# Optimization experiments

Hardware: AMD Instinct MI355X
Metric: run time of the kernel (lower is better)

The kernel has to match this reference:

```python
import jax, jax.numpy as jnp
import numpy as np

B, T, D, H, C = 32, 512, 768, 512, 7


def setup_inputs() -> dict:
    key = jax.random.key(0)
    ks = jax.random.split(key, 10)
    g = lambda k, shape: jax.random.normal(k, shape, jnp.float32) * 0.02
    return {
        "x": jax.random.normal(ks[0], (B, T, D), jnp.float32),
        # PyTorch LSTM params; b = b_ih + b_hh folded into one bias (same math)
        "Wf_ih": g(ks[1], (4 * H, 2 * D)),
        "Wf_hh": g(ks[2], (4 * H, H)),
        "bf": jnp.zeros((4 * H,), jnp.float32),
        "Wb_ih": g(ks[3], (4 * H, 2 * D)),
        "Wb_hh": g(ks[4], (4 * H, H)),
        "bb": jnp.zeros((4 * H,), jnp.float32),
        "W_enc": g(ks[5], (H, D)),
        "b_enc": jnp.zeros((H,), jnp.float32),
        "W_dec": g(ks[6], (H, H)),
        "b_dec": jnp.zeros((H,), jnp.float32),
        "v": jax.random.uniform(ks[7], (H,), jnpp := jnp.float32) if False else jax.random.uniform(ks[7], (H,), jnp.float32),
        "W_head": g(ks[8], (C, 2 * H)),
        "b_head": jnp.zeros((C,), jnp.float32),
    }


def reference(x, Wf_ih, Wf_hh, bf, Wb_ih, Wb_hh, bb, W_enc, b_enc, W_dec, b_dec, v, W_head, b_head):
    hid = W_dec.shape[0]
    # encoder projection is time-invariant -> hoist out of the loop (same math as original)
    enc_proj = jnp.einsum('btd,hd->bth', x, W_enc) + b_enc  # (B,T,H)

    def run_direction(x_seq, Wih, Whh, b):
        def step(carry, xt):
            h, c = carry                                    # (B,H) each
            dec = h @ W_dec.T + b_dec                       # (B,H)
            scores = jnp.tanh(enc_proj + dec[:, None, :]) @ v  # (B,T)
            w = jax.nn.softmax(scores, axis=1)
            ctx = jnp.einsum('bt,btd->bd', w, x)            # (B,D)
            inp = jnp.concatenate([ctx, xt], axis=1)        # (B,2D)
            gates = inp @ Wih.T + h @ Whh.T + b             # (B,4H), torch order i,f,g,o
            i_, f_, g_, o_ = jnp.split(gates, 4, axis=1)
            c = jax.nn.sigmoid(f_) * c + jax.nn.sigmoid(i_) * jnp.tanh(g_)
            h = jax.nn.sigmoid(o_) * jnp.tanh(c)
            return (h, c), h

        h0 = jnp.zeros((x.shape[0], hid), x.dtype)
        (_, _), hs = jax.lax.scan(step, (h0, h0), x_seq)
        return hs                                           # (T,B,H)

    x_seq = jnp.swapaxes(x, 0, 1)                           # (T,B,D)
    hs_f = run_direction(x_seq, Wf_ih, Wf_hh, bf)
    hs_b = run_direction(x_seq[::-1], Wb_ih, Wb_hh, bb)[::-1]
    comb = jnp.swapaxes(jnp.concatenate([hs_f, hs_b], axis=-1), 0, 1)  # (B,T,2H)
    return comb @ W_head.T + b_head                          # (B,T,C)
```

## Files before the change

kernel.cpp:

```cpp
#include <hip/hip_runtime.h>
#include <cstdint>
#include <cstddef>

#define L2E 1.4426950408889634f

typedef __attribute__((ext_vector_type(8))) short short8v;
typedef __attribute__((ext_vector_type(4))) float f32x4;
typedef unsigned long long ull;

__device__ __forceinline__ float fexp2(float x){ return __builtin_amdgcn_exp2f(x); }
__device__ __forceinline__ float frcp(float x){ return __builtin_amdgcn_rcpf(x); }
__device__ __forceinline__ float tanh_f(float x){
  return 1.f - 2.f*frcp(1.f + fexp2(2.f*L2E*x));
}
__device__ __forceinline__ float sigm_f(float x){
  return frcp(1.f + fexp2(-L2E*x));
}
__device__ __forceinline__ float bf2f(ushort u){ return __uint_as_float(((uint32_t)u)<<16); }
__device__ __forceinline__ ushort f2bf(float f){
  uint32_t x = __float_as_uint(f);
  uint32_t r = (x + 0x7FFFu + ((x>>16)&1u)) >> 16;
  return (ushort)r;
}

__device__ __forceinline__ float ld4f(const float* p){
  return __hip_atomic_load((float*)p, __ATOMIC_RELAXED, __HIP_MEMORY_SCOPE_AGENT);
}
__device__ __forceinline__ void st4f(float* p, float v){
  __hip_atomic_store(p, v, __ATOMIC_RELAXED, __HIP_MEMORY_SCOPE_AGENT);
}
__device__ __forceinline__ void st2h(ushort* p, ushort v){
  __hip_atomic_store(p, v, __ATOMIC_RELAXED, __HIP_MEMORY_SCOPE_AGENT);
}
__device__ __forceinline__ short8v ld16h(const ushort* p){
  union { ull u[2]; short8v s; } c;
  c.u[0] = __hip_atomic_load((ull*)p,     __ATOMIC_RELAXED, __HIP_MEMORY_SCOPE_AGENT);
  c.u[1] = __hip_atomic_load((ull*)(p+4), __ATOMIC_RELAXED, __HIP_MEMORY_SCOPE_AGENT);
  return c.s;
}
__device__ __forceinline__ void st8u(ushort* p, ull v){
  __hip_atomic_store((ull*)p, v, __ATOMIC_RELAXED, __HIP_MEMORY_SCOPE_AGENT);
}

namespace {
constexpr int NB = 32, TT = 512, DD = 768, HH = 512;
constexpr size_t EPB  = 0;
constexpr size_t XBB  = EPB  + (size_t)NB*HH*TT*2;
constexpr size_t HSB  = XBB  + (size_t)NB*TT*DD*2;
constexpr size_t WPKB = HSB  + (size_t)2*TT*NB*HH*2;
constexpr size_t WDPB = WPKB + (size_t)2*128*64*64*8*2;
constexpr size_t CTXB = WDPB + (size_t)32*16*64*8*2;
constexpr size_t CSTB = CTXB + (size_t)2*NB*DD*4;
constexpr size_t GSYB = CSTB + (size_t)2*NB*HH*4;
constexpr size_t WS_BYTES = GSYB + 32768;

constexpr int EPL  = 0;
constexpr int WPL  = 65536;
constexpr int REDL = 131072;
constexpr int HEVL = 147456;
constexpr int HBL  = 151680;
constexpr int DPL  = 153856;
constexpr int DECL = 155904;
constexpr int VVL  = 156416;
constexpr int CSCL = 156672;
constexpr int GFNL = 159776;
constexpr int LDS_BYTES = GFNL + 2176;
}

__device__ __forceinline__ void bar_arrive(uint* flags, uint token, int bid){
  __syncthreads();
  if (threadIdx.x == 0)
    __hip_atomic_store(&flags[bid*16], token, __ATOMIC_RELAXED, __HIP_MEMORY_SCOPE_AGENT);
}
__device__ __forceinline__ void bar_wait(uint* flags, uint token){
  if (threadIdx.x < 256) {
    while (__hip_atomic_load(&flags[threadIdx.x*16], __ATOMIC_RELAXED, __HIP_MEMORY_SCOPE_AGENT) < token)
      __builtin_amdgcn_s_sleep(1);
  }
  __syncthreads();
  asm volatile("" ::: "memory");
}

__global__ void k_xcast(const float* __restrict__ x, ushort* __restrict__ xb)
{
  size_t i = ((size_t)blockIdx.x*256 + threadIdx.x)*8;
  float4 v0 = *(const float4*)(x + i);
  float4 v1 = *(const float4*)(x + i + 4);
  short8v o;
  o[0]=(short)f2bf(v0.x); o[1]=(short)f2bf(v0.y); o[2]=(short)f2bf(v0.z); o[3]=(short)f2bf(v0.w);
  o[4]=(short)f2bf(v1.x); o[5]=(short)f2bf(v1.y); o[6]=(short)f2bf(v1.z); o[7]=(short)f2bf(v1.w);
  *(short8v*)(xb + i) = o;
}

__global__ void k_encproj(const float* __restrict__ x, const float* __restrict__ Wenc,
                          const float* __restrict__ benc, ushort* __restrict__ epT)
{
  int b = blockIdx.z, h0 = blockIdx.y*64, t0 = blockIdx.x*64;
  __shared__ float As[64][33];
  __shared__ float Bs[64][33];
  int tid = threadIdx.x;
  int n = tid & 63, mg = tid >> 6;
  float acc[16];
  #pragma unroll
  for (int j = 0; j < 16; j++) acc[j] = 0.f;
  int lr = tid >> 2, lk = (tid & 3) * 8;
  for (int k0 = 0; k0 < 768; k0 += 32) {
    const float* ap = Wenc + (size_t)(h0 + lr)*768 + k0 + lk;
    #pragma unroll
    for (int i = 0; i < 8; i++) As[lr][lk + i] = ap[i];
    const float* bp = x + ((size_t)b*512 + t0 + lr)*768 + k0 + lk;
    #pragma unroll
    for (int i = 0; i < 8; i++) Bs[lr][lk + i] = bp[i];
    __syncthreads();
    #pragma unroll
    for (int kk = 0; kk < 32; kk++) {
      float bv = Bs[n][kk];
      #pragma unroll
      for (int j = 0; j < 16; j++) acc[j] += As[mg*16 + j][kk] * bv;
    }
    __syncthreads();
  }
  #pragma unroll
  for (int j = 0; j < 16; j++) {
    int h = h0 + mg*16 + j;
    epT[((size_t)b*512 + h)*512 + t0 + n] = f2bf(acc[j] + benc[h]);
  }
}

__global__ void k_wpack(const float* __restrict__ Wfih, const float* __restrict__ Wfhh,
                        const float* __restrict__ Wbih, const float* __restrict__ Wbhh,
                        ushort* __restrict__ wpk)
{
  size_t f = (size_t)blockIdx.x*256 + threadIdx.x;
  int lane = (int)(f & 63), kstep = (int)((f>>6)&63), jblk = (int)((f>>12)&127), dir = (int)(f>>19);
  const float* Whh = dir ? Wbhh : Wfhh;
  const float* Wih = dir ? Wbih : Wfih;
  int c = lane & 15, gate = c >> 2, jj = c & 3;
  int row = gate*512 + jblk*4 + jj;
  int kbase = kstep*32 + (lane>>4)*8;
  short8v o;
  #pragma unroll
  for (int i = 0; i < 8; i++) {
    int k = kbase + i;
    float w = (k < 512) ? Whh[(size_t)row*512 + k] : Wih[(size_t)row*1536 + (k - 512)];
    o[i] = (short)f2bf(w);
  }
  *(short8v*)(wpk + f*8) = o;
}

__global__ void k_wdpack(const float* __restrict__ Wdec, ushort* __restrict__ wdp)
{
  int f = blockIdx.x*256 + threadIdx.x;
  int lane = f & 63, kstep = (f >> 6) & 15, nb = f >> 10;
  int n = nb*16 + (lane & 15);
  int kbase = kstep*32 + (lane >> 4)*8;
  short8v o;
  #pragma unroll
  for (int i = 0; i < 8; i++) o[i] = (short)f2bf(Wdec[(size_t)n*512 + kbase + i]);
  *(short8v*)(wdp + (size_t)f*8) = o;
}

__device__ __forceinline__ void gates_hx(int s, int wid, int lane, int l15, int lk8, int dirG,
    const ushort* __restrict__ hsb, const ushort* __restrict__ xb,
    const ushort* wpk_l, float* RED)
{
  if (wid >= 2 && wid <= 4) return;
  int b0 = l15, b1 = 16 + l15;
  f32x4 acc0 = {0,0,0,0}, acc1 = {0,0,0,0};
  if (wid < 2) {
    if (s > 0) {
      int t_prev = dirG ? (512 - s) : (s - 1);
      const ushort* h0 = hsb + (((size_t)dirG*512 + t_prev)*32 + b0)*512;
      const ushort* h1 = hsb + (((size_t)dirG*512 + t_prev)*32 + b1)*512;
      #pragma unroll
      for (int kk = 0; kk < 8; kk++) {
        int kstep = wid*8 + kk;
        int ko = kstep*32 + lk8;
        short8v a0v = *(const short8v*)(h0 + ko);
        short8v a1v = *(const short8v*)(h1 + ko);
        short8v bv  = *(const short8v*)(wpk_l + (size_t)kstep*512 + lane*8);
        acc0 = __builtin_amdgcn_mfma_f32_16x16x32_bf16(a0v, bv, acc0, 0, 0, 0);
        acc1 = __builtin_amdgcn_mfma_f32_16x16x32_bf16(a1v, bv, acc1, 0, 0, 0);
      }
    }
  } else {
    int t_in = dirG ? (511 - s) : s;
    const ushort* x0 = xb + ((size_t)b0*512 + t_in)*768;
    const ushort* x1 = xb + ((size_t)b1*512 + t_in)*768;
    #pragma unroll
    for (int kk = 0; kk < 8; kk++) {
      int kstep = wid*8 + kk;
      int ko = kstep*32 - 1280 + lk8;
      short8v a0v = *(const short8v*)(x0 + ko);
      short8v a1v = *(const short8v*)(x1 + ko);
      short8v bv  = *(const short8v*)(wpk_l + (size_t)kstep*512 + lane*8);
      acc0 = __builtin_amdgcn_mfma_f32_16x16x32_bf16(a0v, bv, acc0, 0, 0, 0);
      acc1 = __builtin_amdgcn_mfma_f32_16x16x32_bf16(a1v, bv, acc1, 0, 0, 0);
    }
  }
  int rr = (lane >> 4) * 4;
  #pragma unroll
  for (int r = 0; r < 4; r++) RED[((size_t)wid*32 + rr + r)*16 + l15] = acc0[r];
  #pragma unroll
  for (int r = 0; r < 4; r++) RED[((size_t)wid*32 + 16 + rr + r)*16 + l15] = acc1[r];
}

__global__ __launch_bounds__(512, 1) void k_loop(
    ushort* __restrict__ hsb, const ushort* __restrict__ xb, const ushort* __restrict__ ep,
    const ushort* __restrict__ wpk, const ushort* __restrict__ wdp,
    float* __restrict__ spart, ushort* __restrict__ ctxf,
    float* __restrict__ cst, const float* __restrict__ bdec, const float* __restrict__ vg,
    const float* __restrict__ bfv, const float* __restrict__ bbv,
    uint* __restrict__ flags, uint* __restrict__ gfl)
{
  extern __shared__ __align__(16) char dsm[];
  ushort* ep_l  = (ushort*)(dsm + EPL);
  ushort* wpk_l = (ushort*)(dsm + WPL);
  float*  RED   = (float*)(dsm + REDL);
  float*  HEV   = (float*)(dsm + HEVL);
  ushort* HB    = (ushort*)(dsm + HBL);
  float*  DP    = (float*)(dsm + DPL);
  float*  DEC   = (float*)(dsm + DECL);
  float*  VV    = (float*)(dsm + VVL);
  float*  CSC   = (float*)(dsm + CSCL);
  float*  GFIN  = (float*)(dsm + GFNL);

  const int bid = blockIdx.x;
  const int tid = threadIdx.x;
  const int wid = tid >> 6, lane = tid & 63;
  const int l15 = lane & 15, lk8 = (lane >> 4) * 8;
  const int bS = bid >> 3, hc = bid & 7;
  const int dirG = bid >> 7, jblkG = bid & 127;
  uint bar_t = 0;

  {
    const short8v* esrc = (const short8v*)(ep + ((size_t)bS*512 + hc*64)*512);
    short8v* edst = (short8v*)ep_l;
    for (int i = tid; i < 4096; i += 512) edst[i] = esrc[i];
    const short8v* wsrc = (const short8v*)(wpk + (((size_t)dirG*128 + jblkG)*64)*512);
    short8v* wdst = (short8v*)wpk_l;
    for (int i = tid; i < 4096; i += 512) wdst[i] = wsrc[i];
    if (tid < 64) VV[tid] = vg[hc*64 + tid];
  }
  ++bar_t; bar_arrive(flags, bar_t, bid); bar_wait(flags, bar_t);

  for (int s = 0; s < TT; ++s) {
    if (s == 0) {
      if (tid < 128) { int dir = tid >> 6, n = tid & 63; DEC[dir*64 + n] = bdec[hc*64 + n]; }
    } else {
      if (tid < 128) {
        int dir = tid >> 6, q = tid & 63;
        int tp = dir ? (512 - s) : (s - 1);
        short8v hv = *(const short8v*)(hsb + (((size_t)dir*512 + tp)*32 + bS)*512 + q*8);
        *(short8v*)&HB[(dir*4 + (q >> 4))*136 + (q & 15)*8] = hv;
      }
      __syncthreads();
      {
        int dir = tid >> 8, n = (tid >> 2) & 63, kq = tid & 3;
        int ng = hc*64 + n, nb = ng >> 4, c = ng & 15;
        const ushort* hrow = HB + (dir*4 + kq)*136;
        float a = 0.f;
        #pragma unroll
        for (int ch = 0; ch < 16; ch++) {
          int kstep = kq*4 + (ch >> 2), lhi = ch & 3;
          short8v w8 = *(const short8v*)(wdp + (((size_t)nb*16 + kstep)*64 + lhi*16 + c)*8);
          #pragma unroll
          for (int j = 0; j < 8; j++) a += bf2f((ushort)w8[j]) * bf2f(hrow[ch*8 + j]);
        }
        DP[tid] = a;
      }
      __syncthreads();
      if (tid < 128) {
        int dir = tid >> 6, n = tid & 63;
        const float* dp = DP + dir*256 + n*4;
        DEC[dir*64 + n] = dp[0] + dp[1] + dp[2] + dp[3] + bdec[hc*64 + n];
      }
    }
    __syncthreads();

    float s0 = 0.f, s1 = 0.f;
    {
      int t = tid;
      #pragma unroll 8
      for (int h = 0; h < 64; h++) {
        float e = bf2f(ep_l[h*512 + t]);
        float vv = VV[h];
        s0 += tanh_f(e + DEC[h]) * vv;
        s1 += tanh_f(e + DEC[64 + h]) * vv;
      }
    }

    {
      float* sp = spart + (((size_t)(bS*8 + hc))*2)*512;
      st4f(sp + tid, s0);
      st4f(sp + 512 + tid, s1);
      __syncthreads();
      if (tid == 0)
        __hip_atomic_store(&gfl[bid*16], (uint)(s + 1), __ATOMIC_RELAXED, __HIP_MEMORY_SCOPE_AGENT);
      if (tid < 8) {
        while (__hip_atomic_load(&gfl[(bS*8 + tid)*16], __ATOMIC_RELAXED, __HIP_MEMORY_SCOPE_AGENT) < (uint)(s + 1))
          __builtin_amdgcn_s_sleep(1);
      }
      __syncthreads();
      float s0r = 0.f, s1r = 0.f;
      #pragma unroll
      for (int j = 0; j < 8; j++) {
        const float* spj = spart + (((size_t)(bS*8 + j))*2)*512;
        s0r += ld4f(spj + tid);
        s1r += ld4f(spj + 512 + tid);
      }
      s0r = fminf(s0r, 100.f); s1r = fminf(s1r, 100.f);
      float e0 = fexp2((s0r - 32.f)*L2E);
      float e1 = fexp2((s1r - 32.f)*L2E);
      float z0 = e0, z1 = e1;
      #pragma unroll
      for (int off = 32; off; off >>= 1) { z0 += __shfl_xor(z0, off); z1 += __shfl_xor(z1, off); }
      if (lane == 0) { DP[wid] = z0; DP[8 + wid] = z1; }
      __syncthreads();
      if (tid < 2) {
        float z = 0.f;
        #pragma unroll
        for (int w = 0; w < 8; w++) z += DP[tid*8 + w];
        DP[128 + tid] = frcp(z);
      }
      __syncthreads();
      e0 *= DP[128]; e1 *= DP[129];
      HEV[(tid >> 7)*132 + (tid & 127)] = e0;
      HEV[(4 + (tid >> 7))*132 + (tid & 127)] = e1;
      __syncthreads();
    }

    if (tid < 384) {
      int dl = tid % 96, tq = tid / 96;
      const ushort* xp = xb + (((size_t)bS*512 + tq*128)*768) + hc*96 + dl;
      const float* ev0 = HEV + tq*132;
      const float* ev1 = HEV + (4 + tq)*132;
      float a0 = 0.f, a1 = 0.f;
      #pragma unroll 8
      for (int t2 = 0; t2 < 128; t2++) {
        float xv = bf2f(xp[(size_t)t2*768]);
        a0 += ev0[t2]*xv;
        a1 += ev1[t2]*xv;
      }
      CSC[(tq*2 + 0)*97 + dl] = a0;
      CSC[(tq*2 + 1)*97 + dl] = a1;
    }
    __syncthreads();
    if (tid < 192) {
      int dl = tid % 96, dir = tid / 96;
      float cv = CSC[(0*2 + dir)*97 + dl] + CSC[(1*2 + dir)*97 + dl]
               + CSC[(2*2 + dir)*97 + dl] + CSC[(3*2 + dir)*97 + dl];
      st2h(ctxf + ((size_t)dir*32 + bS)*768 + hc*96 + dl, f2bf(cv));
    }

    ++bar_t; bar_arrive(flags, bar_t, bid);
    gates_hx(s, wid, lane, l15, lk8, dirG, hsb, xb, wpk_l, RED);
    bar_wait(flags, bar_t);

    {
      if (wid >= 2 && wid <= 4) {
        int b0 = l15, b1 = 16 + l15;
        f32x4 acc0 = {0,0,0,0}, acc1 = {0,0,0,0};
        const ushort* c0 = ctxf + ((size_t)dirG*32 + b0)*768;
        const ushort* c1 = ctxf + ((size_t)dirG*32 + b1)*768;
        #pragma unroll
        for (int kk = 0; kk < 8; kk++) {
          int kstep = wid*8 + kk;
          int ko = kstep*32 - 512 + lk8;
          short8v a0v = ld16h(c0 + ko);
          short8v a1v = ld16h(c1 + ko);
          short8v bv  = *(const short8v*)(wpk_l + (size_t)kstep*512 + lane*8);
          acc0 = __builtin_amdgcn_mfma_f32_16x16x32_bf16(a0v, bv, acc0, 0, 0, 0);
          acc1 = __builtin_amdgcn_mfma_f32_16x16x32_bf16(a1v, bv, acc1, 0, 0, 0);
        }
        int rr = (lane >> 4) * 4;
        #pragma unroll
        for (int r = 0; r < 4; r++) RED[((size_t)wid*32 + rr + r)*16 + l15] = acc0[r];
        #pragma unroll
        for (int r = 0; r < 4; r++) RED[((size_t)wid*32 + 16 + rr + r)*16 + l15] = acc1[r];
      }
      __syncthreads();
      {
        int bb = tid >> 4, c = tid & 15;
        float g = 0.f;
        #pragma unroll
        for (int w = 0; w < 8; w++) g += RED[((size_t)w*32 + bb)*16 + c];
        GFIN[bb*17 + c] = g;
      }
      __syncthreads();
      if (tid < 32) {
        int b = tid;
        int j0 = jblkG*4;
        const float* bias = dirG ? bbv : bfv;
        size_t ci0 = ((size_t)dirG*32 + b)*512 + j0;
        float4 co = *(const float4*)&cst[ci0];
        float cold[4] = {co.x, co.y, co.z, co.w};
        float4 cn4;
        ull hp = 0;
        #pragma unroll
        for (int jj = 0; jj < 4; jj++) {
          int j = j0 + jj;
          float gi  = GFIN[b*17 + jj]       + bias[j];
          float gf  = GFIN[b*17 + 4 + jj]   + bias[512 + j];
          float gg  = GFIN[b*17 + 8 + jj]   + bias[1024 + j];
          float go_ = GFIN[b*17 + 12 + jj]  + bias[1536 + j];
          float cn = sigm_f(gf)*cold[jj] + sigm_f(gi)*tanh_f(gg);
          float h  = sigm_f(go_)*tanh_f(cn);
          ((float*)&cn4)[jj] = cn;
          hp |= ((ull)f2bf(h)) << (16*jj);
        }
        *(float4*)&cst[ci0] = cn4;
        int tw = dirG ? (511 - s) : s;
        st8u(hsb + (((size_t)dirG*512 + tw)*32 + b)*512 + j0, hp);
      }
    }
    ++bar_t; bar_arrive(flags, bar_t, bid);
    bar_wait(flags, bar_t);
  }
}

__global__ void k_head(const ushort* __restrict__ hsb, const float* __restrict__ Wh,
                       const float* __restrict__ bh, float* __restrict__ out)
{
  int wid = threadIdx.x >> 6, lane = threadIdx.x & 63;
  int r = blockIdx.x*4 + wid;
  int b = r >> 9, t = r & 511;
  float acc[7];
  #pragma unroll
  for (int c = 0; c < 7; c++) acc[c] = 0.f;
  const ushort* hf = hsb + (((size_t)t)*32 + b)*512;
  const ushort* hb = hsb + (((size_t)512 + t)*32 + b)*512;
  for (int k0 = 0; k0 < 512; k0 += 64) {
    int k = k0 + lane;
    float a = bf2f(hf[k]), bvv = bf2f(hb[k]);
    #pragma unroll
    for (int c = 0; c < 7; c++)
      acc[c] += a*Wh[c*1024 + k] + bvv*Wh[c*1024 + 512 + k];
  }
  #pragma unroll
  for (int c = 0; c < 7; c++) {
    float sres = acc[c];
    #pragma unroll
    for (int off = 32; off; off >>= 1) sres += __shfl_xor(sres, off);
    if (lane == c) out[((size_t)b*512 + t)*7 + c] = sres + bh[c];
  }
}

extern "C" void kernel_launch(void* const* d_in, const int* in_sizes, int n_in,
                              void* d_out, int out_size, void* d_ws, size_t ws_size,
                              hipStream_t stream) {
  (void)in_sizes; (void)n_in; (void)out_size;
  const float* x    = (const float*)d_in[0];
  const float* Wfih = (const float*)d_in[1];
  const float* Wfhh = (const float*)d_in[2];
  const float* bfv  = (const float*)d_in[3];
  const float* Wbih = (const float*)d_in[4];
  const float* Wbhh = (const float*)d_in[5];
  const float* bbv  = (const float*)d_in[6];
  const float* Wenc = (const float*)d_in[7];
  const float* benc = (const float*)d_in[8];
  const float* Wdec = (const float*)d_in[9];
  const float* bdec = (const float*)d_in[10];
  const float* v    = (const float*)d_in[11];
  const float* Whead= (const float*)d_in[12];
  const float* bhead= (const float*)d_in[13];
  float* out = (float*)d_out;
  char* ws = (char*)d_ws;

  if (ws_size < WS_BYTES) return;

  ushort* ep   = (ushort*)(ws + EPB);
  float*  spart= (float*)(ws + EPB);
  ushort* xb   = (ushort*)(ws + XBB);
  ushort* hsb  = (ushort*)(ws + HSB);
  ushort* wpk  = (ushort*)(ws + WPKB);
  ushort* wdp  = (ushort*)(ws + WDPB);
  ushort* ctxf = (ushort*)(ws + CTXB);
  float*  cst  = (float*)(ws + CSTB);
  uint*   flags= (uint*)(ws + GSYB);
  uint*   gfl  = (uint*)(ws + GSYB + 16384);

  hipFuncSetAttribute(reinterpret_cast<const void*>(k_loop),
                      hipFuncAttributeMaxDynamicSharedMemorySize, LDS_BYTES);

  hipMemsetAsync(ws + CSTB, 0, (size_t)2*NB*HH*4, stream);
  hipMemsetAsync(ws + GSYB, 0, 32768, stream);

  hipLaunchKernelGGL(k_xcast, dim3(6144), dim3(256), 0, stream, x, xb);
  hipLaunchKernelGGL(k_encproj, dim3(8,8,32), dim3(256), 0, stream, x, Wenc, benc, ep);
  hipLaunchKernelGGL(k_wpack, dim3(4096), dim3(256), 0, stream, Wfih, Wfhh, Wbih, Wbhh, wpk);
  hipLaunchKernelGGL(k_wdpack, dim3(128), dim3(256), 0, stream, Wdec, wdp);

  void* args[] = {
    (void*)&hsb, (void*)&xb, (void*)&ep, (void*)&wpk, (void*)&wdp,
    (void*)&spart, (void*)&ctxf, (void*)&cst,
    (void*)&bdec, (void*)&v, (void*)&bfv, (void*)&bbv,
    (void*)&flags, (void*)&gfl
  };
  hipLaunchCooperativeKernel(reinterpret_cast<void*>(k_loop), dim3(256), dim3(512),
                             args, LDS_BYTES, stream);

  hipLaunchKernelGGL(k_head, dim3(4096), dim3(256), 0, stream, hsb, Whead, bhead, out);
}
```

Measured before the change: 14.01 ms.

## Split gate GEMM into h and x parts and overlap each with barrier waits

The fused h/x gate GEMM is split into two functions. The input-x contribution for step s+1 is now computed while waiting on the end-of-step grid barrier, including once before the loop for step 0. The recurrent h contribution is computed while waiting on the score-partial flags, with the spin-waiting threads moved to wave 2 so waves 0-1 can run the MFMAs. The aim is to hide GEMM latency behind the grid-wide synchronisation stalls. It relies on RED slots for x and h waves not being overwritten between producer and consumer across barriers.

Result: slower. 14.87 ms (+6.2%).

```diff
diff --git a/kernel.cpp b/kernel.cpp
--- a/kernel.cpp
+++ b/kernel.cpp
@@ -160,43 +160,52 @@
   *(short8v*)(wdp + (size_t)f*8) = o;
 }
 
-__device__ __forceinline__ void gates_hx(int s, int wid, int lane, int l15, int lk8, int dirG,
-    const ushort* __restrict__ hsb, const ushort* __restrict__ xb,
-    const ushort* wpk_l, float* RED)
-{
-  if (wid >= 2 && wid <= 4) return;
+__device__ __forceinline__ void gates_h(int s, int wid, int lane, int l15, int lk8, int dirG,
+    const ushort* __restrict__ hsb, const ushort* wpk_l, float* RED)
+{
+  if (wid >= 2) return;
   int b0 = l15, b1 = 16 + l15;
   f32x4 acc0 = {0,0,0,0}, acc1 = {0,0,0,0};
-  if (wid < 2) {
-    if (s > 0) {
-      int t_prev = dirG ? (512 - s) : (s - 1);
-      const ushort* h0 = hsb + (((size_t)dirG*512 + t_prev)*32 + b0)*512;
-      const ushort* h1 = hsb + (((size_t)dirG*512 + t_prev)*32 + b1)*512;
-      #pragma unroll
-      for (int kk = 0; kk < 8; kk++) {
-        int kstep = wid*8 + kk;
-        int ko = kstep*32 + lk8;
-        short8v a0v = *(const short8v*)(h0 + ko);
-        short8v a1v = *(const short8v*)(h1 + ko);
-        short8v bv  = *(const short8v*)(wpk_l + (size_t)kstep*512 + lane*8);
-        acc0 = __builtin_amdgcn_mfma_f32_16x16x32_bf16(a0v, bv, acc0, 0, 0, 0);
-        acc1 = __builtin_amdgcn_mfma_f32_16x16x32_bf16(a1v, bv, acc1, 0, 0, 0);
-      }
-    }
-  } else {
-    int t_in = dirG ? (511 - s) : s;
-    const ushort* x0 = xb + ((size_t)b0*512 + t_in)*768;
-    const ushort* x1 = xb + ((size_t)b1*512 + t_in)*768;
+  if (s > 0) {
+    int t_prev = dirG ? (512 - s) : (s - 1);
+    const ushort* h0 = hsb + (((size_t)dirG*512 + t_prev)*32 + b0)*512;
+    const ushort* h1 = hsb + (((size_t)dirG*512 + t_prev)*32 + b1)*512;
     #pragma unroll
     for (int kk = 0; kk < 8; kk++) {
       int kstep = wid*8 + kk;
-      int ko = kstep*32 - 1280 + lk8;
-      short8v a0v = *(const short8v*)(x0 + ko);
-      short8v a1v = *(const short8v*)(x1 + ko);
+      int ko = kstep*32 + lk8;
+      short8v a0v = *(const short8v*)(h0 + ko);
+      short8v a1v = *(const short8v*)(h1 + ko);
       short8v bv  = *(const short8v*)(wpk_l + (size_t)kstep*512 + lane*8);
       acc0 = __builtin_amdgcn_mfma_f32_16x16x32_bf16(a0v, bv, acc0, 0, 0, 0);
       acc1 = __builtin_amdgcn_mfma_f32_16x16x32_bf16(a1v, bv, acc1, 0, 0, 0);
     }
+  }
+  int rr = (lane >> 4) * 4;
+  #pragma unroll
+  for (int r = 0; r < 4; r++) RED[((size_t)wid*32 + rr + r)*16 + l15] = acc0[r];
+  #pragma unroll
+  for (int r = 0; r < 4; r++) RED[((size_t)wid*32 + 16 + rr + r)*16 + l15] = acc1[r];
+}
+
+__device__ __forceinline__ void gates_x(int s, int wid, int lane, int l15, int lk8, int dirG,
+    const ushort* __restrict__ xb, const ushort* wpk_l, float* RED)
+{
+  if (wid < 5) return;
+  int b0 = l15, b1 = 16 + l15;
+  f32x4 acc0 = {0,0,0,0}, acc1 = {0,0,0,0};
+  int t_in = dirG ? (511 - s) : s;
+  const ushort* x0 = xb + ((size_t)b0*512 + t_in)*768;
+  const ushort* x1 = xb + ((size_t)b1*512 + t_in)*768;
+  #pragma unroll
+  for (int kk = 0; kk < 8; kk++) {
+    int kstep = wid*8 + kk;
+    int ko = kstep*32 - 1280 + lk8;
+    short8v a0v = *(const short8v*)(x0 + ko);
+    short8v a1v = *(const short8v*)(x1 + ko);
+    short8v bv  = *(const short8v*)(wpk_l + (size_t)kstep*512 + lane*8);
+    acc0 = __builtin_amdgcn_mfma_f32_16x16x32_bf16(a0v, bv, acc0, 0, 0, 0);
+    acc1 = __builtin_amdgcn_mfma_f32_16x16x32_bf16(a1v, bv, acc1, 0, 0, 0);
   }
   int rr = (lane >> 4) * 4;
   #pragma unroll
@@ -242,7 +251,9 @@
     for (int i = tid; i < 4096; i += 512) wdst[i] = wsrc[i];
     if (tid < 64) VV[tid] = vg[hc*64 + tid];
   }
-  ++bar_t; bar_arrive(flags, bar_t, bid); bar_wait(flags, bar_t);
+  ++bar_t; bar_arrive(flags, bar_t, bid);
+  gates_x(0, wid, lane, l15, lk8, dirG, xb, wpk_l, RED);
+  bar_wait(flags, bar_t);
 
   for (int s = 0; s < TT; ++s) {
     if (s == 0) {
@@ -297,8 +308,9 @@
       __syncthreads();
       if (tid == 0)
         __hip_atomic_store(&gfl[bid*16], (uint)(s + 1), __ATOMIC_RELAXED, __HIP_MEMORY_SCOPE_AGENT);
-      if (tid < 8) {
-        while (__hip_atomic_load(&gfl[(bS*8 + tid)*16], __ATOMIC_RELAXED, __HIP_MEMORY_SCOPE_AGENT) < (uint)(s + 1))
+      gates_h(s, wid, lane, l15, lk8, dirG, hsb, wpk_l, RED);
+      if (tid >= 128 && tid < 136) {
+        while (__hip_atomic_load(&gfl[(bS*8 + (tid - 128))*16], __ATOMIC_RELAXED, __HIP_MEMORY_SCOPE_AGENT) < (uint)(s + 1))
           __builtin_amdgcn_s_sleep(1);
       }
       __syncthreads();
@@ -354,7 +366,6 @@
     }
 
     ++bar_t; bar_arrive(flags, bar_t, bid);
-    gates_hx(s, wid, lane, l15, lk8, dirG, hsb, xb, wpk_l, RED);
     bar_wait(flags, bar_t);
 
     {
@@ -415,6 +426,8 @@
       }
     }
     ++bar_t; bar_arrive(flags, bar_t, bid);
+    if (s + 1 < TT)
+      gates_x(s + 1, wid, lane, l15, lk8, dirG, xb, wpk_l, RED);
     bar_wait(flags, bar_t);
   }
 }
```
